# Optimization experiments

Hardware: AMD Instinct MI355X
Metric: run time of the kernel (lower is better)

Reference implementation:

```python
import jax, jax.numpy as jnp
import numpy as np
from jax import lax

GATE_SLOPE = 10.0
ALPHA = 0.8
B, IN_DIM, OUT_DIM, NUM_BASIS = 256, 128, 128, 16


def setup_inputs() -> dict:
    key = jax.random.key(0)
    k1, k2, k3, k4, k5, k6 = jax.random.split(key, 6)
    pshape = (IN_DIM, OUT_DIM, NUM_BASIS)
    return {
        "x": jax.random.normal(k1, (B, IN_DIM), dtype=jnp.float32),
        "k": jax.random.uniform(k2, pshape, dtype=jnp.float32) * 2.0 + 0.5,
        "Ec": jax.random.uniform(k3, pshape, dtype=jnp.float32) * 2.0 + 0.5,
        "Ps": jax.random.uniform(k4, pshape, dtype=jnp.float32) * 1.5 + 0.5,
        "bias": jax.random.normal(k5, pshape, dtype=jnp.float32) * 0.1,
        "coef": jax.random.normal(k6, pshape, dtype=jnp.float32),
    }


def reference(x, k, Ec, Ps, bias, coef):
    # Sequential hysteresis over the batch dimension (lax.scan replaces the
    # per-sample Python loop). Carry: (prev_x, branch_sign), each [in,out,nb].
    pshape = k.shape  # (in_dim, out_dim, num_basis)

    def step(carry, xb):
        prev_x, bs = carry
        xs = xb[:, None, None]                       # [in,1,1] broadcasts to pshape
        dx = xs - prev_x
        is_up = jax.nn.sigmoid(GATE_SLOPE * dx)
        crossed_pos = jax.nn.sigmoid(GATE_SLOPE * (xs - Ec))
        crossed_neg = jax.nn.sigmoid(GATE_SLOPE * (-xs - Ec))
        su = is_up * crossed_pos
        sl = (1.0 - is_up) * crossed_neg
        target = su - sl + (1.0 - su - sl) * bs
        bs_new = ALPHA * bs + (1.0 - ALPHA) * target
        basis = Ps * jnp.tanh(k * (xs + Ec * bs_new)) + bias
        # torch does prev_x.copy_(x_sample.detach()) -> stop_gradient
        prev_x_new = lax.stop_gradient(jnp.broadcast_to(xs, pshape))
        return (prev_x_new, bs_new), basis

    init = (jnp.zeros(pshape, x.dtype), jnp.ones(pshape, x.dtype))
    _, basis_all = lax.scan(step, init, x)            # [B,in,out,nb]
    # weighted sum over in_dim and num_basis -> [B, out_dim]
    output = jnp.einsum('bion,ion->bo', basis_all, coef)
    return output
```

## Files before the change

kernel.cpp:

```cpp
#include <hip/hip_runtime.h>

#define GATE_SLOPE 10.0f
#define ALPHA 0.8f
constexpr int B_ = 256, IN_DIM = 128, OUT_DIM = 128, NB = 16;

__device__ __forceinline__ float rcpf(float x)  { return __builtin_amdgcn_rcpf(x); }
__device__ __forceinline__ float ex2f(float x)  { return __builtin_amdgcn_exp2f(x); }

template<int CTRL>
__device__ __forceinline__ float dpp_add(float v) {
    int s = __builtin_amdgcn_update_dpp(0, __builtin_bit_cast(int, v),
                                        CTRL, 0xF, 0xF, true);
    return v + __builtin_bit_cast(float, s);
}

__launch_bounds__(256, 4)
__global__ void ferro_kernel(const float* __restrict__ x,
                             const float* __restrict__ k,
                             const float* __restrict__ Ec,
                             const float* __restrict__ Ps,
                             const float* __restrict__ bias,
                             const float* __restrict__ coef,
                             float* __restrict__ target,
                             int repmask)
{
    constexpr float LOG2E = 1.4426950408889634f;
    constexpr float S = GATE_SLOPE * LOG2E;

    __shared__ float4 st[B_];

    const int t   = threadIdx.x;
    const int blk = blockIdx.x;
    const int i      = blk >> 3;
    const int o_base = (blk & 7) << 4;

    {
        float xb = x[t * IN_DIM + i];
        float xp = (t == 0) ? 0.0f : x[(t - 1) * IN_DIM + i];
        float up = rcpf(1.0f + ex2f((xp - xb) * S));
        float upA = 0.2f * up;
        st[t] = make_float4(xb, upA, 0.2f - upA, ex2f(-xb * S));
    }
    __syncthreads();

    const long pidx = (long)i * (OUT_DIM * NB) + (long)o_base * NB + t;
    const float kk = k[pidx];
    const float ec = Ec[pidx];
    const float ps = Ps[pidx];
    const float bi = bias[pidx];
    const float cf = coef[pidx];

    const int o = o_base + (t >> 4);
    const int n = t & 15;

    const float ecS   = ec * S;
    const float E1c   = ex2f(ecS);
    const float E2c   = ex2f(2.0f * ecS);
    const float kt    = kk * (2.0f * LOG2E);
    const float ktec  = kt * ec;
    const float psc   = ps * cf;
    const float m2psc = -2.0f * psc;
    const float pbc   = __builtin_fmaf(bi, cf, psc);

    float* __restrict__ rbase = target + ((long)(i & repmask) << 15);

    float bs = 1.0f;

    for (int b0 = 0; b0 < B_; b0 += 8) {
        float AA[8], CC[8], KX[8];
        #pragma unroll
        for (int u = 0; u < 8; ++u) {
            const float4 s4 = st[b0 + u];
            const float e1  = E1c * s4.w;
            const float r1  = rcpf(1.0f + e1);
            const float r2  = rcpf(e1 + E2c);
            const float su2 = s4.y * r1;
            const float sl2 = (s4.z * e1) * r2;
            AA[u] = 1.0f - (su2 + sl2);
            CC[u] = su2 - sl2;
            KX[u] = kt * s4.x;
        }
        __builtin_amdgcn_sched_barrier(0);
        #pragma unroll
        for (int u = 0; u < 8; ++u) {
            bs = __builtin_fmaf(AA[u], bs, CC[u]);
            const float zk = __builtin_fmaf(ktec, bs, KX[u]);
            const float e3 = ex2f(zk);
            const float r3 = rcpf(1.0f + e3);
            float v = __builtin_fmaf(m2psc, r3, pbc);
            v = dpp_add<0xB1>(v);
            v = dpp_add<0x4E>(v);
            v = dpp_add<0x141>(v);
            v = dpp_add<0x140>(v);
            if (n == 0) atomicAdd(&rbase[((b0 + u) << 7) + o], v);
        }
    }
}

__global__ void reduce_kernel(const float* __restrict__ ws,
                              float* __restrict__ out, int R)
{
    const int j = blockIdx.x * blockDim.x + threadIdx.x;
    float s = 0.0f;
    for (int r = 0; r < R; ++r) s += ws[((long)r << 15) + j];
    out[j] = s;
}

extern "C" void kernel_launch(void* const* d_in, const int* in_sizes, int n_in,
                              void* d_out, int out_size, void* d_ws, size_t ws_size,
                              hipStream_t stream) {
    const float* x    = (const float*)d_in[0];
    const float* k    = (const float*)d_in[1];
    const float* Ec   = (const float*)d_in[2];
    const float* Ps   = (const float*)d_in[3];
    const float* bias = (const float*)d_in[4];
    const float* coef = (const float*)d_in[5];
    float* out = (float*)d_out;
    float* ws  = (float*)d_ws;

    const size_t repBytes = (size_t)32768 * sizeof(float);
    int R = 0;
    if (ws_size >= repBytes) {
        R = 1;
        while (R < 16 && (size_t)(R * 2) * repBytes <= ws_size) R <<= 1;
    }

    if (R >= 2) {
        hipMemsetAsync(ws, 0, (size_t)R * repBytes, stream);
        ferro_kernel<<<dim3(IN_DIM * 8), dim3(256), 0, stream>>>(
            x, k, Ec, Ps, bias, coef, ws, R - 1);
        reduce_kernel<<<dim3(128), dim3(256), 0, stream>>>(ws, out, R);
    } else {
        hipMemsetAsync(out, 0, (size_t)out_size * sizeof(float), stream);
        ferro_kernel<<<dim3(IN_DIM * 8), dim3(256), 0, stream>>>(
            x, k, Ec, Ps, bias, coef, out, 0);
    }
}
```

Baseline: 134.6 us.

## Software-pipeline gate computation one chunk ahead of the serial recurrence

Restructures the batch loop into a two-stage software pipeline. The gate coefficients for the next 8-sample chunk are computed while the current chunk's serial recurrence and outputs run. Empty asm constraints pin the arrays in registers, and the shared table is padded so the last prefetch reads valid dummy values. Each chunk's outputs are batched so the 8 exp/rcp evaluations, the DPP reductions and the atomics issue back to back instead of interleaved. This is meant to hide transcendental latency behind the bs dependency chain, at the cost of higher VGPR pressure that may hurt occupancy under launch_bounds(256,4).

```diff
diff --git a/kernel.cpp b/kernel.cpp
--- a/kernel.cpp
+++ b/kernel.cpp
@@ -3,6 +3,7 @@
 #define GATE_SLOPE 10.0f
 #define ALPHA 0.8f
 constexpr int B_ = 256, IN_DIM = 128, OUT_DIM = 128, NB = 16;
+constexpr int BPAD = 16;
 
 __device__ __forceinline__ float rcpf(float x)  { return __builtin_amdgcn_rcpf(x); }
 __device__ __forceinline__ float ex2f(float x)  { return __builtin_amdgcn_exp2f(x); }
@@ -13,6 +14,53 @@
                                         CTRL, 0xF, 0xF, true);
     return v + __builtin_bit_cast(float, s);
 }
+
+#define PIN8(A) asm volatile("" : "+v"(A[0]), "+v"(A[1]), "+v"(A[2]), \
+    "+v"(A[3]), "+v"(A[4]), "+v"(A[5]), "+v"(A[6]), "+v"(A[7]))
+
+#define GATES(b0, AA, CC, KX)                                         \
+    do {                                                              \
+        _Pragma("unroll")                                             \
+        for (int u = 0; u < 8; ++u) {                                 \
+            const float4 s4 = st[(b0) + u];            \
+            const float e1  = E1c * s4.w;        \
+            const float ra  = rcpf(1.0f + e1);                \
+            const float rb  = rcpf(e1 + E2c);                         \
+            const float su2 = s4.y * ra;               \
+            const float sl2 = (s4.z * e1) * rb;    \
+            AA[u] = 1.0f - (su2 + sl2);                               \
+            CC[u] = su2 - sl2;                                        \
+            KX[u] = kt * s4.x;                                        \
+        }                                                             \
+    } while (0)
+
+#define OUTPUTS(b0, AA, CC, KX)                                       \
+    do {                                                              \
+        float ZK[8];                                                  \
+        _Pragma("unroll")                                             \
+        for (int u = 0; u < 8; ++u) {                                 \
+            bs = __builtin_fmaf(AA[u], bs, CC[u]);                    \
+            ZK[u] = __builtin_fmaf(ktec, bs, KX[u]);                  \
+        }                                                             \
+        float VV[8];                                                  \
+        _Pragma("unroll")                                             \
+        for (int u = 0; u < 8; ++u)                                   \
+            VV[u] = __builtin_fmaf(m2psc, rcpf(1.0f + ex2f(ZK[u])), pbc); \
+        _Pragma("unroll")                                             \
+        for (int u = 0; u < 8; ++u) {                                 \
+            float v = VV[u];                                          \
+            v = dpp_add<0xB1>(v);                          \
+            v = dpp_add<0x4E>(v);                          \
+            v = dpp_add<0x141>(v);                         \
+            v = dpp_add<0x140>(v);                        \
+            VV[u] = v;                                                \
+        }                                                             \
+        if (n == 0) {                                                 \
+            _Pragma("unroll")                                         \
+            for (int u = 0; u < 8; ++u)                               \
+                atomicAdd(&rbase[(((b0) + u) << 7) + o], VV[u]);      \
+        }                                                             \
+    } while (0)
 
 __launch_bounds__(256, 4)
 __global__ void ferro_kernel(const float* __restrict__ x,
@@ -27,7 +75,7 @@
     constexpr float LOG2E = 1.4426950408889634f;
     constexpr float S = GATE_SLOPE * LOG2E;
 
-    __shared__ float4 st[B_];
+    __shared__ float4 st[B_ + BPAD];
 
     const int t   = threadIdx.x;
     const int blk = blockIdx.x;
@@ -40,6 +88,7 @@
         float up = rcpf(1.0f + ex2f((xp - xb) * S));
         float upA = 0.2f * up;
         st[t] = make_float4(xb, upA, 0.2f - upA, ex2f(-xb * S));
+        if (t < BPAD) st[B_ + t] = make_float4(0.0f, 0.1f, 0.1f, 1.0f);
     }
     __syncthreads();
 
@@ -66,34 +115,13 @@
 
     float bs = 1.0f;
 
-    for (int b0 = 0; b0 < B_; b0 += 8) {
-        float AA[8], CC[8], KX[8];
-        #pragma unroll
-        for (int u = 0; u < 8; ++u) {
-            const float4 s4 = st[b0 + u];
-            const float e1  = E1c * s4.w;
-            const float r1  = rcpf(1.0f + e1);
-            const float r2  = rcpf(e1 + E2c);
-            const float su2 = s4.y * r1;
-            const float sl2 = (s4.z * e1) * r2;
-            AA[u] = 1.0f - (su2 + sl2);
-            CC[u] = su2 - sl2;
-            KX[u] = kt * s4.x;
-        }
-        __builtin_amdgcn_sched_barrier(0);
-        #pragma unroll
-        for (int u = 0; u < 8; ++u) {
-            bs = __builtin_fmaf(AA[u], bs, CC[u]);
-            const float zk = __builtin_fmaf(ktec, bs, KX[u]);
-            const float e3 = ex2f(zk);
-            const float r3 = rcpf(1.0f + e3);
-            float v = __builtin_fmaf(m2psc, r3, pbc);
-            v = dpp_add<0xB1>(v);
-            v = dpp_add<0x4E>(v);
-            v = dpp_add<0x141>(v);
-            v = dpp_add<0x140>(v);
-            if (n == 0) atomicAdd(&rbase[((b0 + u) << 7) + o], v);
-        }
+    float A0[8], C0[8], K0[8], A1[8], C1[8], K1[8];
+    GATES(0, A0, C0, K0);  PIN8(A0); PIN8(C0); PIN8(K0);
+    for (int b0 = 0; b0 < B_; b0 += 16) {
+        GATES(b0 + 8, A1, C1, K1);  PIN8(A1); PIN8(C1); PIN8(K1);
+        OUTPUTS(b0, A0, C0, K0);
+        GATES(b0 + 16, A0, C0, K0); PIN8(A0); PIN8(C0); PIN8(K0);
+        OUTPUTS(b0 + 8, A1, C1, K1);
     }
 }
 
```

Result: faster. 131.6 us (-2.2%).
